# Optimization experiments

Measured on AMD Instinct MI355X. Metric: run time of the kernel, lower is better.

Reference implementation:

```python
import jax, jax.numpy as jnp
import numpy as np
from jax import lax

SLOPE = 0.1  # LeakyRelu(0.1)
DN = ('NCHW', 'OIHW', 'NCHW')


def _xavier(key, shape, cin, cout):
    bound = 2.0 / (cout + cin) ** 0.5
    return jax.random.uniform(key, shape, jnp.float32, -bound, bound)


def setup_inputs() -> dict:
    key = jax.random.key(0)
    ks = jax.random.split(key, 9)
    x = jax.random.normal(ks[0], (8, 3, 256, 256), jnp.float32)
    # Conv2d always adds bias in forward (even with bias=False flag), so biases included.
    w1 = _xavier(ks[1], (48, 3, 3, 3), 3, 48)
    b1 = _xavier(ks[2], (48,), 3, 48)
    w2 = _xavier(ks[3], (48, 48, 3, 3), 48, 48)
    b2 = _xavier(ks[4], (48,), 48, 48)
    w3 = _xavier(ks[5], (48, 48, 3, 3), 48, 48)
    b3 = _xavier(ks[6], (48,), 48, 48)
    w4 = _xavier(ks[7], (48, 48, 3, 3), 48, 48)
    b4 = _xavier(ks[8], (48,), 48, 48)
    return {"x": x, "w1": w1, "b1": b1, "w2": w2, "b2": b2,
            "w3": w3, "b3": b3, "w4": w4, "b4": b4}


def _convblock(x, w, b):
    # 3x3 stride-1 pad-1 conv (original does unfold + matmul; math identical)
    y = lax.conv_general_dilated(x, w, (1, 1), [(1, 1), (1, 1)], dimension_numbers=DN)
    y = y + b[None, :, None, None]
    # LeakyReLU: x * (mask*(1-s)+s) == where(x>0, x, s*x)
    return jnp.where(y > 0, y, SLOPE * y)


def _maxpool2(x):
    n, c, h, w = x.shape
    return x.reshape(n, c, h // 2, 2, w // 2, 2).max(axis=(3, 5))


def reference(x, w1, b1, w2, b2, w3, b3, w4, b4):
    # encoder01: conv(3->48) + conv(48->48) + maxpool
    h = _convblock(x, w1, b1)
    h = _convblock(h, w2, b2)
    h = _maxpool2(h)
    # encoder2: conv(48->48) + maxpool
    h = _convblock(h, w3, b3)
    h = _maxpool2(h)
    # encoder3: conv(48->48) + maxpool
    h = _convblock(h, w4, b4)
    h = _maxpool2(h)
    return h  # (8, 48, 32, 32)
```

## Files before the change

kernel.cpp:

```cpp
#include <hip/hip_runtime.h>
#include <hip/hip_bf16.h>

typedef _Float16 half_t;
typedef _Float16 f16x8 __attribute__((ext_vector_type(8)));
typedef _Float16 f16x4 __attribute__((ext_vector_type(4)));
typedef float f32x4 __attribute__((ext_vector_type(4)));

#define LEAKY 0.1f

__global__ __launch_bounds__(512) void prep_w_k(const float* __restrict__ w2,
                                                const float* __restrict__ w3,
                                                const float* __restrict__ w4,
                                                half_t* __restrict__ wp234)
{
    int t = blockIdx.x * 512 + threadIdx.x;
    if (t >= 3 * 23040) return;
    int layer = t / 23040;
    int r = t % 23040;
    int tap = r / 2304;
    int r2 = r % 2304;
    int co = r2 / 48, ci = r2 % 48;
    const float* src = layer == 0 ? w2 : (layer == 1 ? w3 : w4);
    float v = 0.f;
    if (tap < 9) v = src[((co * 48 + ci) * 3 + tap / 3) * 3 + tap % 3];
    wp234[t] = (half_t)v;
}

__global__ __launch_bounds__(256, 3) void conv12_k(const float* __restrict__ x,
                                                   const float* __restrict__ w1,
                                                   const float* __restrict__ b1,
                                                   const half_t* __restrict__ wp2,
                                                   const float* __restrict__ b2,
                                                   half_t* __restrict__ out)
{
    __shared__ alignas(16) half_t in_t[352 * 56];
    __shared__ alignas(16) half_t xt[13][36][4];
    __shared__ alignas(16) half_t w1t[48 * 40];

    const int tid = threadIdx.x;
    const int n = blockIdx.z;
    const int hblk = blockIdx.x * 8, wblk = blockIdx.y * 32;
    const int lane = tid & 63, hp = tid >> 6;
    const int m = lane & 15, g = lane >> 4;

    for (int t = tid; t < 1920; t += 256) {
        int co = t / 40, kk = t % 40;
        float v = 0.f;
        if (kk < 27) {
            int tap = kk / 3, ci = kk % 3;
            v = w1[((co * 3 + ci) * 3 + tap / 3) * 3 + tap % 3];
        }
        w1t[t] = (half_t)v;
    }
    for (int c = tid; c < 1404; c += 256) {
        int ci = c / 468, rem = c % 468;
        int row = rem / 36, col = rem % 36;
        int gh = hblk - 2 + row, gw = wblk - 2 + col;
        float v = 0.f;
        if ((unsigned)gh < 256u && (unsigned)gw < 256u)
            v = x[((n * 3 + ci) * 256 + gh) * 256 + gw];
        xt[row][col][ci] = (half_t)v;
    }
    __syncthreads();

    int xoff[8];
    #pragma unroll
    for (int j = 0; j < 8; ++j) {
        int k = g * 8 + j;
        int tap = k / 3, ci = k - 3 * tap;
        int dr = tap / 3, ds = tap - 3 * dr;
        xoff[j] = (k < 27) ? ((dr * 36 + ds) * 8 + ci * 2) : 0;
    }
    f16x8 wf[3];
    float bb1[12];
    #pragma unroll
    for (int nt = 0; nt < 3; ++nt) {
        wf[nt] = *(const f16x8*)((const char*)w1t + (nt * 16 + m) * 80 + g * 16);
        #pragma unroll
        for (int j = 0; j < 4; ++j) bb1[nt * 4 + j] = b1[nt * 16 + 4 * g + j];
    }
    const char* xtb = (const char*)&xt[0][0][0];
    #pragma unroll
    for (int tt = 0; tt < 6; ++tt) {
        int t = hp + tt * 4;
        if (t < 22) {
            int px = t * 16 + m;
            int row = px / 34, col = px - row * 34;
            int pxb = (row * 36 + col) * 8;
            f16x8 pf;
            #pragma unroll
            for (int j = 0; j < 8; ++j)
                pf[j] = *(const half_t*)(xtb + pxb + xoff[j]);
            bool inb = ((unsigned)(hblk - 1 + row) < 256u) && ((unsigned)(wblk - 1 + col) < 256u);
            #pragma unroll
            for (int nt = 0; nt < 3; ++nt) {
                f32x4 d = {0.f, 0.f, 0.f, 0.f};
                d = __builtin_amdgcn_mfma_f32_16x16x32_f16(wf[nt], pf, d, 0, 0, 0);
                f16x4 o;
                #pragma unroll
                for (int j = 0; j < 4; ++j) {
                    float v = d[j] + bb1[nt * 4 + j];
                    v = v > 0.f ? v : LEAKY * v;
                    o[j] = inb ? (half_t)v : (half_t)0.f;
                }
                *(f16x4*)(&in_t[px * 56 + nt * 16 + 4 * g]) = o;
            }
        }
    }
    __syncthreads();

    const int hpar = m & 1, wloc = m >> 1;
    const int abase = hp * 2 * 34 * 112;
    const char* ib = (const char*)&in_t[0];
    const char* bp = (const char*)wp2 + m * 96;

    f32x4 acc[4][3];
    #pragma unroll
    for (int mt = 0; mt < 4; ++mt)
        #pragma unroll
        for (int nt = 0; nt < 3; ++nt)
            acc[mt][nt] = (f32x4){0.f, 0.f, 0.f, 0.f};

    #pragma unroll
    for (int s = 0; s < 14; ++s) {
        int kc = 4 * s + g;
        int tap = kc / 6, ci8 = kc - tap * 6;
        int dr = tap / 3, ds = tap - 3 * dr;
        if (tap == 9) { dr = 0; ds = 0; }
        int aoff = ((hpar + dr) * 34 + (wloc + ds)) * 112 + ci8 * 16;
        int boff = tap * 4608 + ci8 * 16;
        f16x8 b0 = *(const f16x8*)(bp + boff);
        f16x8 b1f = *(const f16x8*)(bp + boff + 1536);
        f16x8 b2f = *(const f16x8*)(bp + boff + 3072);
        f16x8 a[4];
        #pragma unroll
        for (int mt = 0; mt < 4; ++mt)
            a[mt] = *(const f16x8*)(ib + abase + aoff + mt * 896);
        __builtin_amdgcn_s_setprio(1);
        #pragma unroll
        for (int mt = 0; mt < 4; ++mt) {
            acc[mt][0] = __builtin_amdgcn_mfma_f32_16x16x32_f16(a[mt], b0, acc[mt][0], 0, 0, 0);
            acc[mt][1] = __builtin_amdgcn_mfma_f32_16x16x32_f16(a[mt], b1f, acc[mt][1], 0, 0, 0);
            acc[mt][2] = __builtin_amdgcn_mfma_f32_16x16x32_f16(a[mt], b2f, acc[mt][2], 0, 0, 0);
        }
        __builtin_amdgcn_s_setprio(0);
    }

    int hq = blockIdx.x * 4 + hp;
    #pragma unroll
    for (int nt = 0; nt < 3; ++nt) {
        int co = nt * 16 + m;
        float bb = b2[co];
        #pragma unroll
        for (int mt = 0; mt < 4; ++mt) {
            float pmax = -1e30f;
            #pragma unroll
            for (int j = 0; j < 4; ++j) {
                float v = acc[mt][nt][j] + bb;
                v = v > 0.f ? v : LEAKY * v;
                pmax = fmaxf(pmax, v);
            }
            int wq = blockIdx.y * 16 + mt * 4 + g;
            out[((n * 128 + hq) * 128 + wq) * 48 + co] = (half_t)pmax;
        }
    }
}

template<int H, int W, int MT, int NTS, bool FINAL>
__global__ __launch_bounds__(256, 4)
void convpool4_k(const half_t* __restrict__ in,
                 const half_t* __restrict__ wp,
                 const float* __restrict__ bias,
                 void* __restrict__ outv)
{
    constexpr int HO = H / 2, WO = W / 2;
    constexpr int TC = 8 * MT + 2;
    constexpr int NU4 = 10 * TC * 6;

    __shared__ alignas(16) half_t in_t[10][TC][56];

    int tid = threadIdx.x;
    int n = blockIdx.z & 7, ntb = blockIdx.z >> 3;
    int hblk = blockIdx.x * 8, wblk = blockIdx.y * (8 * MT);
    int lane = tid & 63, hp = tid >> 6;
    int m = lane & 15, g = lane >> 4;
    int hpar = m & 1, wloc = m >> 1;

    {
        const uint4* s4 = (const uint4*)in;
        uint4* d = (uint4*)&in_t[0][0][0];
        #pragma unroll
        for (int i = 0; i < (NU4 + 255) / 256; ++i) {
            int c = tid + i * 256;
            if (c < NU4) {
                int row = c / (TC * 6);
                int rem = c - row * (TC * 6);
                int pix = rem / 6;
                int sub = rem - pix * 6;
                int gh = hblk - 1 + row, gw = wblk - 1 + pix;
                uint4 v = {0u, 0u, 0u, 0u};
                if ((unsigned)gh < (unsigned)H && (unsigned)gw < (unsigned)W)
                    v = s4[((n * H + gh) * W + gw) * 6 + sub];
                d[(row * TC + pix) * 7 + sub] = v;
            }
        }
    }

    int abase = hp * 2 * TC * 112;
    const char* ib = (const char*)&in_t[0][0][0];
    const char* bp = (const char*)wp + m * 96 + ntb * NTS * 1536;

    f32x4 acc[MT][NTS];
    #pragma unroll
    for (int mt = 0; mt < MT; ++mt)
        #pragma unroll
        for (int nt = 0; nt < NTS; ++nt)
            acc[mt][nt] = (f32x4){0.f, 0.f, 0.f, 0.f};

    __syncthreads();

    #pragma unroll
    for (int s = 0; s < 14; ++s) {
        int kc = 4 * s + g;
        int tap = kc / 6, ci8 = kc - tap * 6;
        int dr = tap / 3, ds = tap - 3 * dr;
        if (tap == 9) { dr = 0; ds = 0; }
        int aoff = ((hpar + dr) * TC + (wloc + ds)) * 112 + ci8 * 16;
        int boff = tap * 4608 + ci8 * 16;
        f16x8 bfrag[NTS];
        #pragma unroll
        for (int nt = 0; nt < NTS; ++nt)
            bfrag[nt] = *(const f16x8*)(bp + boff + nt * 1536);
        f16x8 a[MT];
        #pragma unroll
        for (int mt = 0; mt < MT; ++mt)
            a[mt] = *(const f16x8*)(ib + abase + aoff + mt * 896);
        __builtin_amdgcn_s_setprio(1);
        #pragma unroll
        for (int mt = 0; mt < MT; ++mt)
            #pragma unroll
            for (int nt = 0; nt < NTS; ++nt)
                acc[mt][nt] = __builtin_amdgcn_mfma_f32_16x16x32_f16(a[mt], bfrag[nt], acc[mt][nt], 0, 0, 0);
        __builtin_amdgcn_s_setprio(0);
    }

    int hq = blockIdx.x * 4 + hp;
    #pragma unroll
    for (int nt = 0; nt < NTS; ++nt) {
        int co = (ntb * NTS + nt) * 16 + m;
        float bb = bias[co];
        #pragma unroll
        for (int mt = 0; mt < MT; ++mt) {
            float pmax = -1e30f;
            #pragma unroll
            for (int j = 0; j < 4; ++j) {
                float v = acc[mt][nt][j] + bb;
                v = v > 0.f ? v : LEAKY * v;
                pmax = fmaxf(pmax, v);
            }
            int wq = blockIdx.y * (4 * MT) + mt * 4 + g;
            if (FINAL)
                ((float*)outv)[(((long)n * 48 + co) * HO + hq) * WO + wq] = pmax;
            else
                ((half_t*)outv)[((n * HO + hq) * WO + wq) * 48 + co] = (half_t)pmax;
        }
    }
}

extern "C" void kernel_launch(void* const* d_in, const int* in_sizes, int n_in,
                              void* d_out, int out_size, void* d_ws, size_t ws_size,
                              hipStream_t stream)
{
    const float* x  = (const float*)d_in[0];
    const float* w1 = (const float*)d_in[1];
    const float* b1 = (const float*)d_in[2];
    const float* w2 = (const float*)d_in[3];
    const float* b2 = (const float*)d_in[4];
    const float* w3 = (const float*)d_in[5];
    const float* b3 = (const float*)d_in[6];
    const float* w4 = (const float*)d_in[7];
    const float* b4 = (const float*)d_in[8];

    half_t* Wb = (half_t*)d_ws;
    half_t* wp2  = Wb;
    half_t* wp3  = wp2 + 23040;
    half_t* wp4  = wp3 + 23040;
    half_t* act2 = Wb + 69120;
    half_t* act3 = act2 + 6291456;

    prep_w_k<<<dim3(135), 512, 0, stream>>>(w2, w3, w4, wp2);

    conv12_k<<<dim3(32, 8, 8), 256, 0, stream>>>(x, w1, b1, wp2, b2, act2);
    convpool4_k<128, 128, 4, 3, false><<<dim3(16, 4, 8), 256, 0, stream>>>(act2, wp3, b3, act3);
    convpool4_k<64, 64, 2, 1, true><<<dim3(8, 4, 24), 256, 0, stream>>>(act3, wp4, b4, d_out);
}
```

Before: 68.81 us.

## Enlarge conv12 tiles, repack weights per-lane, fold w3/w4 prep into conv12

The fused conv1+conv2 kernel now works on 16-row tiles with 512 threads per block, which cuts the halo recompute of conv1 per output. Weight packing is reordered so each lane's three B fragments are contiguous (m*48 stride), and the conv2 inner loop double-buffers B fragment loads across K steps. Preparation of the w3/w4 weights moves out of the prep kernel into conv12's blocks, and w1 is prepacked by prep_w_k and then copied into LDS. The larger LDS footprint and 512-thread blocks may reduce occupancy.

```diff
diff --git a/kernel.cpp b/kernel.cpp
--- a/kernel.cpp
+++ b/kernel.cpp
@@ -8,52 +8,77 @@
 
 #define LEAKY 0.1f
 
-__global__ __launch_bounds__(512) void prep_w_k(const float* __restrict__ w2,
-                                                const float* __restrict__ w3,
-                                                const float* __restrict__ w4,
-                                                half_t* __restrict__ wp234)
+__global__ __launch_bounds__(512) void prep_w_k(const float* __restrict__ w1,
+                                                const float* __restrict__ w2,
+                                                half_t* __restrict__ wp1,
+                                                half_t* __restrict__ wp2)
 {
     int t = blockIdx.x * 512 + threadIdx.x;
-    if (t >= 3 * 23040) return;
-    int layer = t / 23040;
-    int r = t % 23040;
-    int tap = r / 2304;
-    int r2 = r % 2304;
-    int co = r2 / 48, ci = r2 % 48;
-    const float* src = layer == 0 ? w2 : (layer == 1 ? w3 : w4);
-    float v = 0.f;
-    if (tap < 9) v = src[((co * 48 + ci) * 3 + tap / 3) * 3 + tap % 3];
-    wp234[t] = (half_t)v;
-}
-
-__global__ __launch_bounds__(256, 3) void conv12_k(const float* __restrict__ x,
-                                                   const float* __restrict__ w1,
-                                                   const float* __restrict__ b1,
-                                                   const half_t* __restrict__ wp2,
-                                                   const float* __restrict__ b2,
-                                                   half_t* __restrict__ out)
-{
-    __shared__ alignas(16) half_t in_t[352 * 56];
-    __shared__ alignas(16) half_t xt[13][36][4];
-    __shared__ alignas(16) half_t w1t[48 * 40];
-
-    const int tid = threadIdx.x;
-    const int n = blockIdx.z;
-    const int hblk = blockIdx.x * 8, wblk = blockIdx.y * 32;
-    const int lane = tid & 63, hp = tid >> 6;
-    const int m = lane & 15, g = lane >> 4;
-
-    for (int t = tid; t < 1920; t += 256) {
+    if (t < 1920) {
         int co = t / 40, kk = t % 40;
         float v = 0.f;
         if (kk < 27) {
             int tap = kk / 3, ci = kk % 3;
             v = w1[((co * 3 + ci) * 3 + tap / 3) * 3 + tap % 3];
         }
-        w1t[t] = (half_t)v;
-    }
-    for (int c = tid; c < 1404; c += 256) {
-        int ci = c / 468, rem = c % 468;
+        wp1[t] = (half_t)v;
+        return;
+    }
+    int t2 = t - 1920;
+    if (t2 >= 23040) return;
+    int tap = t2 / 2304, r = t2 % 2304;
+    int ci8 = r / 384, r2 = r % 384;
+    int mm = r2 / 24, r3 = r2 % 24;
+    int nt = r3 / 8, j = r3 % 8;
+    int co = nt * 16 + mm, ci = ci8 * 8 + j;
+    float v = 0.f;
+    if (tap < 9) v = w2[((co * 48 + ci) * 3 + tap / 3) * 3 + tap % 3];
+    wp2[t2] = (half_t)v;
+}
+
+__global__ __launch_bounds__(512, 4) void conv12_k(const float* __restrict__ x,
+                                                   const half_t* __restrict__ wp1,
+                                                   const float* __restrict__ b1,
+                                                   const half_t* __restrict__ wp2,
+                                                   const float* __restrict__ b2,
+                                                   const float* __restrict__ w3,
+                                                   const float* __restrict__ w4,
+                                                   half_t* __restrict__ wp34,
+                                                   half_t* __restrict__ out)
+{
+    __shared__ alignas(16) half_t in_t[624 * 56];
+    __shared__ alignas(16) half_t xt[21][36][4];
+    __shared__ alignas(16) half_t w1t[1920];
+
+    const int tid = threadIdx.x;
+    const int n = blockIdx.z;
+    const int hblk = blockIdx.x * 16, wblk = blockIdx.y * 32;
+    const int lane = tid & 63, hp = tid >> 6;
+    const int m = lane & 15, g = lane >> 4;
+
+    {
+        int bid = blockIdx.x + 16 * (blockIdx.y + 8 * blockIdx.z);
+        int t2 = bid * 512 + tid;
+        if (t2 < 46080) {
+            int layer = t2 / 23040, r0 = t2 % 23040;
+            int tap = r0 / 2304, r = r0 % 2304;
+            int ci8 = r / 384, r2 = r % 384;
+            int mm = r2 / 24, r3 = r2 % 24;
+            int nt = r3 / 8, j = r3 % 8;
+            int co = nt * 16 + mm, ci = ci8 * 8 + j;
+            const float* src = layer ? w4 : w3;
+            float v = 0.f;
+            if (tap < 9) v = src[((co * 48 + ci) * 3 + tap / 3) * 3 + tap % 3];
+            wp34[t2] = (half_t)v;
+        }
+    }
+    {
+        const uint4* s = (const uint4*)wp1;
+        uint4* d = (uint4*)w1t;
+        if (tid < 240) d[tid] = s[tid];
+    }
+    for (int c = tid; c < 2268; c += 512) {
+        int ci = c / 756, rem = c % 756;
         int row = rem / 36, col = rem % 36;
         int gh = hblk - 2 + row, gw = wblk - 2 + col;
         float v = 0.f;
@@ -76,43 +101,40 @@
     #pragma unroll
     for (int nt = 0; nt < 3; ++nt) {
         wf[nt] = *(const f16x8*)((const char*)w1t + (nt * 16 + m) * 80 + g * 16);
-        #pragma unroll
-        for (int j = 0; j < 4; ++j) bb1[nt * 4 + j] = b1[nt * 16 + 4 * g + j];
+        float4 bv = *(const float4*)(b1 + nt * 16 + 4 * g);
+        bb1[nt * 4 + 0] = bv.x; bb1[nt * 4 + 1] = bv.y;
+        bb1[nt * 4 + 2] = bv.z; bb1[nt * 4 + 3] = bv.w;
     }
     const char* xtb = (const char*)&xt[0][0][0];
-    #pragma unroll
-    for (int tt = 0; tt < 6; ++tt) {
-        int t = hp + tt * 4;
-        if (t < 22) {
-            int px = t * 16 + m;
-            int row = px / 34, col = px - row * 34;
-            int pxb = (row * 36 + col) * 8;
-            f16x8 pf;
+    for (int t = hp; t < 39; t += 8) {
+        int px = t * 16 + m;
+        int row = px / 34, col = px - row * 34;
+        int pxb = (row * 36 + col) * 8;
+        f16x8 pf;
+        #pragma unroll
+        for (int j = 0; j < 8; ++j)
+            pf[j] = *(const half_t*)(xtb + pxb + xoff[j]);
+        bool inb = ((unsigned)(hblk - 1 + row) < 256u) && ((unsigned)(wblk - 1 + col) < 256u);
+        #pragma unroll
+        for (int nt = 0; nt < 3; ++nt) {
+            f32x4 d = {0.f, 0.f, 0.f, 0.f};
+            d = __builtin_amdgcn_mfma_f32_16x16x32_f16(wf[nt], pf, d, 0, 0, 0);
+            f16x4 o;
             #pragma unroll
-            for (int j = 0; j < 8; ++j)
-                pf[j] = *(const half_t*)(xtb + pxb + xoff[j]);
-            bool inb = ((unsigned)(hblk - 1 + row) < 256u) && ((unsigned)(wblk - 1 + col) < 256u);
-            #pragma unroll
-            for (int nt = 0; nt < 3; ++nt) {
-                f32x4 d = {0.f, 0.f, 0.f, 0.f};
-                d = __builtin_amdgcn_mfma_f32_16x16x32_f16(wf[nt], pf, d, 0, 0, 0);
-                f16x4 o;
-                #pragma unroll
-                for (int j = 0; j < 4; ++j) {
-                    float v = d[j] + bb1[nt * 4 + j];
-                    v = v > 0.f ? v : LEAKY * v;
-                    o[j] = inb ? (half_t)v : (half_t)0.f;
-                }
-                *(f16x4*)(&in_t[px * 56 + nt * 16 + 4 * g]) = o;
+            for (int j = 0; j < 4; ++j) {
+                float v = d[j] + bb1[nt * 4 + j];
+                v = v > 0.f ? v : LEAKY * v;
+                o[j] = inb ? (half_t)v : (half_t)0.f;
             }
+            *(f16x4*)(&in_t[px * 56 + nt * 16 + 4 * g]) = o;
         }
     }
     __syncthreads();
 
     const int hpar = m & 1, wloc = m >> 1;
-    const int abase = hp * 2 * 34 * 112;
-    const char* ib = (const char*)&in_t[0];
-    const char* bp = (const char*)wp2 + m * 96;
+    const int abase = hp * 7616;
+    const char* ib = (const char*)in_t;
+    const char* bp = (const char*)wp2 + m * 48;
 
     f32x4 acc[4][3];
     #pragma unroll
@@ -121,32 +143,48 @@
         for (int nt = 0; nt < 3; ++nt)
             acc[mt][nt] = (f32x4){0.f, 0.f, 0.f, 0.f};
 
-    #pragma unroll
-    for (int s = 0; s < 14; ++s) {
-        int kc = 4 * s + g;
-        int tap = kc / 6, ci8 = kc - tap * 6;
-        int dr = tap / 3, ds = tap - 3 * dr;
-        if (tap == 9) { dr = 0; ds = 0; }
-        int aoff = ((hpar + dr) * 34 + (wloc + ds)) * 112 + ci8 * 16;
-        int boff = tap * 4608 + ci8 * 16;
-        f16x8 b0 = *(const f16x8*)(bp + boff);
-        f16x8 b1f = *(const f16x8*)(bp + boff + 1536);
-        f16x8 b2f = *(const f16x8*)(bp + boff + 3072);
-        f16x8 a[4];
-        #pragma unroll
-        for (int mt = 0; mt < 4; ++mt)
-            a[mt] = *(const f16x8*)(ib + abase + aoff + mt * 896);
-        __builtin_amdgcn_s_setprio(1);
-        #pragma unroll
-        for (int mt = 0; mt < 4; ++mt) {
-            acc[mt][0] = __builtin_amdgcn_mfma_f32_16x16x32_f16(a[mt], b0, acc[mt][0], 0, 0, 0);
-            acc[mt][1] = __builtin_amdgcn_mfma_f32_16x16x32_f16(a[mt], b1f, acc[mt][1], 0, 0, 0);
-            acc[mt][2] = __builtin_amdgcn_mfma_f32_16x16x32_f16(a[mt], b2f, acc[mt][2], 0, 0, 0);
-        }
-        __builtin_amdgcn_s_setprio(0);
-    }
-
-    int hq = blockIdx.x * 4 + hp;
+    f16x8 bf[2][3], af[4];
+
+#define BLOAD(S, P) { \
+    int kc = 4 * (S) + g; int tap = kc / 6, ci8 = kc - tap * 6; \
+    int boff = tap * 4608 + ci8 * 768; \
+    bf[P][0] = *(const f16x8*)(bp + boff); \
+    bf[P][1] = *(const f16x8*)(bp + boff + 16); \
+    bf[P][2] = *(const f16x8*)(bp + boff + 32); }
+#define ALOAD(S) { \
+    int kc = 4 * (S) + g; int tap = kc / 6, ci8 = kc - tap * 6; \
+    int dr = tap / 3, ds = tap - 3 * dr; \
+    if (tap == 9) { dr = 0; ds = 0; } \
+    int aoff = ((hpar + dr) * 34 + (wloc + ds)) * 112 + ci8 * 16 + abase; \
+    af[0] = *(const f16x8*)(ib + aoff); \
+    af[1] = *(const f16x8*)(ib + aoff + 896); \
+    af[2] = *(const f16x8*)(ib + aoff + 1792); \
+    af[3] = *(const f16x8*)(ib + aoff + 2688); }
+#define MM(P) { \
+    __builtin_amdgcn_s_setprio(1); \
+    _Pragma("unroll") \
+    for (int mt = 0; mt < 4; ++mt) { \
+        acc[mt][0] = __builtin_amdgcn_mfma_f32_16x16x32_f16(af[mt], bf[P][0], acc[mt][0], 0, 0, 0); \
+        acc[mt][1] = __builtin_amdgcn_mfma_f32_16x16x32_f16(af[mt], bf[P][1], acc[mt][1], 0, 0, 0); \
+        acc[mt][2] = __builtin_amdgcn_mfma_f32_16x16x32_f16(af[mt], bf[P][2], acc[mt][2], 0, 0, 0); \
+    } \
+    __builtin_amdgcn_s_setprio(0); }
+
+    BLOAD(0, 0);
+    #pragma unroll
+    for (int ss = 0; ss < 7; ++ss) {
+        BLOAD(2 * ss + 1, 1);
+        ALOAD(2 * ss);
+        MM(0);
+        if (ss < 6) BLOAD(2 * ss + 2, 0);
+        ALOAD(2 * ss + 1);
+        MM(1);
+    }
+#undef BLOAD
+#undef ALOAD
+#undef MM
+
+    int hq = blockIdx.x * 8 + hp;
     #pragma unroll
     for (int nt = 0; nt < 3; ++nt) {
         int co = nt * 16 + m;
@@ -208,7 +246,7 @@
 
     int abase = hp * 2 * TC * 112;
     const char* ib = (const char*)&in_t[0][0][0];
-    const char* bp = (const char*)wp + m * 96 + ntb * NTS * 1536;
+    const char* bp = (const char*)wp + m * 48;
 
     f32x4 acc[MT][NTS];
     #pragma unroll
@@ -226,11 +264,11 @@
         int dr = tap / 3, ds = tap - 3 * dr;
         if (tap == 9) { dr = 0; ds = 0; }
         int aoff = ((hpar + dr) * TC + (wloc + ds)) * 112 + ci8 * 16;
-        int boff = tap * 4608 + ci8 * 16;
+        int boff = tap * 4608 + ci8 * 768;
         f16x8 bfrag[NTS];
         #pragma unroll
         for (int nt = 0; nt < NTS; ++nt)
-            bfrag[nt] = *(const f16x8*)(bp + boff + nt * 1536);
+            bfrag[nt] = *(const f16x8*)(bp + boff + (ntb * NTS + nt) * 16);
         f16x8 a[MT];
         #pragma unroll
         for (int mt = 0; mt < MT; ++mt)
@@ -282,15 +320,15 @@
     const float* b4 = (const float*)d_in[8];
 
     half_t* Wb = (half_t*)d_ws;
-    half_t* wp2  = Wb;
-    half_t* wp3  = wp2 + 23040;
-    half_t* wp4  = wp3 + 23040;
-    half_t* act2 = Wb + 69120;
+    half_t* wp1  = Wb;
+    half_t* wp2  = Wb + 2048;
+    half_t* wp34 = wp2 + 23040;
+    half_t* act2 = wp34 + 46080;
     half_t* act3 = act2 + 6291456;
 
-    prep_w_k<<<dim3(135), 512, 0, stream>>>(w2, w3, w4, wp2);
-
-    conv12_k<<<dim3(32, 8, 8), 256, 0, stream>>>(x, w1, b1, wp2, b2, act2);
-    convpool4_k<128, 128, 4, 3, false><<<dim3(16, 4, 8), 256, 0, stream>>>(act2, wp3, b3, act3);
-    convpool4_k<64, 64, 2, 1, true><<<dim3(8, 4, 24), 256, 0, stream>>>(act3, wp4, b4, d_out);
+    prep_w_k<<<dim3(49), 512, 0, stream>>>(w1, w2, wp1, wp2);
+
+    conv12_k<<<dim3(16, 8, 8), 512, 0, stream>>>(x, wp1, b1, wp2, b2, w3, w4, wp34, act2);
+    convpool4_k<128, 128, 4, 3, false><<<dim3(16, 4, 8), 256, 0, stream>>>(act2, wp34, b3, act3);
+    convpool4_k<64, 64, 2, 1, true><<<dim3(8, 4, 24), 256, 0, stream>>>(act3, wp34 + 23040, b4, d_out);
 }
```

Result: faster. 57.74 us (-16.1%).
